# Optimization experiments

Hardware: AMD Instinct MI355X
Metric: run time of the kernel (lower is better)

The kernel has to match this reference:

```python
import jax, jax.numpy as jnp
import numpy as np

B, T = 64, 64
H = 256
CLIP = 0.2


def _conv(x, W, b, s):
    y = jax.lax.conv_general_dilated(x, W, (s, s), 'VALID',
                                     dimension_numbers=('NHWC', 'HWIO', 'NHWC'))
    return jax.nn.leaky_relu(y + b, negative_slope=0.2)


def _lstm(x, Wk, Wr, b):
    # keras LSTM, gate order i,f,g,o; x: (B,T,256) -> (B,T,256)
    h0 = jnp.zeros((x.shape[0], H), x.dtype)

    def step(carry, xt):
        h, c = carry
        z = xt @ Wk + h @ Wr + b
        i, f, g, o = jnp.split(z, 4, axis=-1)
        c = jax.nn.sigmoid(f) * c + jax.nn.sigmoid(i) * jnp.tanh(g)
        h = jax.nn.sigmoid(o) * jnp.tanh(c)
        return (h, c), h

    _, hs = jax.lax.scan(step, (h0, h0), jnp.swapaxes(x, 0, 1))
    return jnp.swapaxes(hs, 0, 1)


def setup_inputs():
    key = jax.random.key(0)
    ks = jax.random.split(key, 24)
    s = 0.05
    x = jax.random.normal(ks[0], (B, T, 13, 8, 8), jnp.float32)
    a_taken = jax.random.randint(ks[1], (B, T), 0, 36)
    mask = jax.random.randint(ks[2], (B, T, 4096), 0, 2).astype(jnp.int32)
    # taken actions must be legal (mask=1), as in real rollouts
    bi = jnp.repeat(jnp.arange(B), T)
    ti = jnp.tile(jnp.arange(T), B)
    mask = mask.at[bi, ti, a_taken.reshape(-1)].set(1)
    lg_prob_old = -jnp.abs(jax.random.normal(ks[3], (B, T), jnp.float32)) - 1.0
    GAE = jax.random.normal(ks[4], (B, T), jnp.float32)
    old_v_pred = jax.random.normal(ks[5], (B, T), jnp.float32)
    returns = jax.random.normal(ks[6], (B, T), jnp.float32)
    return {
        'x': x, 'mask': mask, 'lg_prob_old': lg_prob_old, 'a_taken': a_taken,
        'GAE': GAE, 'old_v_pred': old_v_pred, 'returns': returns,
        'W1': jax.random.normal(ks[7], (2, 2, 8, 16), jnp.float32) * s,
        'b1': jnp.zeros((16,), jnp.float32),
        'W2': jax.random.normal(ks[8], (2, 2, 16, 32), jnp.float32) * s,
        'b2': jnp.zeros((32,), jnp.float32),
        'W3': jax.random.normal(ks[9], (2, 2, 32, 64), jnp.float32) * s,
        'b3': jnp.zeros((64,), jnp.float32),
        'W4': jax.random.normal(ks[10], (1, 1, 64, 128), jnp.float32) * s,
        'b4': jnp.zeros((128,), jnp.float32),
        'lstm_k': jax.random.normal(ks[11], (256, 1024), jnp.float32) * s,
        'lstm_r': jax.random.normal(ks[12], (256, 1024), jnp.float32) * s,
        'lstm_b': jnp.zeros((1024,), jnp.float32),
        'pir_W': jax.random.normal(ks[13], (256, 36), jnp.float32) * s,
        'pir_b': jnp.zeros((36,), jnp.float32),
        'pim_W': jax.random.normal(ks[14], (256, 4096), jnp.float32) * s,
        'pim_b': jnp.zeros((4096,), jnp.float32),
        'v_W': jax.random.normal(ks[15], (256, 1), jnp.float32) * s,
        'v_b': jnp.zeros((1,), jnp.float32),
    }


def reference(x, mask, lg_prob_old, a_taken, GAE, old_v_pred, returns,
              W1, b1, W2, b2, W3, b3, W4, b4,
              lstm_k, lstm_r, lstm_b, pir_W, pir_b, pim_W, pim_b, v_W, v_b):
    Bn, Tn = x.shape[0], x.shape[1]
    h = x.reshape(Bn * Tn, 13, 8, 8)  # NHWC: H=13, W=8, C=8
    h = _conv(h, W1, b1, 2)  # (BT,6,4,16)
    h = _conv(h, W2, b2, 1)  # (BT,5,3,32)
    h = _conv(h, W3, b3, 2)  # (BT,2,1,64)
    h = _conv(h, W4, b4, 1)  # (BT,2,1,128)
    # keras Flatten(data_format='channels_first') permutes dim1 to last then flattens
    h = jnp.transpose(h, (0, 2, 3, 1)).reshape(Bn, Tn, -1)  # (B,T,256)
    lstm = _lstm(h, lstm_k, lstm_r, lstm_b).reshape(-1, H)  # (BT,256)

    pir = jax.nn.softmax(lstm @ pir_W + pir_b, axis=-1)  # (BT,36)
    maskf = mask.reshape(-1, 4096).astype(jnp.float32)
    pim = jax.nn.softmax(lstm @ pim_W + pim_b, axis=-1) * maskf
    scale = jnp.sum(pim, axis=1, keepdims=True)
    pim = pim / jnp.where(scale > 0, scale, jnp.ones_like(scale))  # (BT,4096)
    vpred = lstm @ v_W + v_b  # (BT,1)

    lg_old = lg_prob_old.reshape(-1)
    a = a_taken.reshape(-1)
    gae = GAE.reshape(-1)
    ovp = old_v_pred.reshape(-1)
    ret = returns.reshape(-1)
    gae = (gae - jnp.mean(gae)) / (jnp.std(gae) + 1e-8)

    t = jnp.arange(a.shape[0])
    p = jnp.where(t % 2 == 0, pir[t, a], pim[t, a])  # alternating heads
    lg_new = jnp.log(p)
    rt = jnp.exp(lg_new - lg_old)
    pg1 = -gae * rt
    pg2 = -gae * jnp.clip(rt, 1.0 - CLIP, 1.0 + CLIP)
    pg_loss = jnp.mean(jnp.maximum(pg1, pg2))

    # faithful to original TF: (BT,1) vpred broadcast against (BT,) -> (BT,BT)
    vpredclipped = ovp + jnp.clip(vpred - ovp, -CLIP, CLIP)
    vf1 = jnp.square(vpred - ret)
    vf2 = jnp.square(vpredclipped - ret)
    vf_loss = 0.5 * jnp.mean(jnp.maximum(vf1, vf2))

    pim_e = pim + (1.0 - maskf)
    entropy = -jnp.sum(pir * jnp.log(pir)) - jnp.sum(pim_e * jnp.log(pim_e))
    loss = pg_loss - entropy + vf_loss
    return (loss, pg_loss, entropy, vf_loss)
```

## Files before the change

### kernel.cpp

```cpp
#include <hip/hip_runtime.h>

typedef unsigned short u16;
typedef unsigned int   u32;

#define BT   4096
#define TSEQ 64
#define NB   64

typedef __attribute__((ext_vector_type(8))) short  short8;
typedef __attribute__((ext_vector_type(4))) float  f32x4;
typedef __attribute__((ext_vector_type(4))) int    i32x4;
typedef __attribute__((ext_vector_type(2))) _Float16 h2;

__device__ __forceinline__ float bf(u16 v) {
    u32 u = ((u32)v) << 16;
    return __builtin_bit_cast(float, u);
}
__device__ __forceinline__ u16 f2b(float f) {
    u32 u = __builtin_bit_cast(u32, f);
    return (u16)((u + 0x7fffu + ((u >> 16) & 1u)) >> 16);
}
__device__ __forceinline__ float lrelu(float x) { return x > 0.f ? x : 0.2f * x; }
__device__ __forceinline__ h2 i2h(int v) { return __builtin_bit_cast(h2, v); }
__device__ __forceinline__ float dot2(int hbits, int wbits, float acc) {
#if __has_builtin(__builtin_amdgcn_fdot2)
    return __builtin_amdgcn_fdot2(i2h(hbits), i2h(wbits), acc, false);
#else
    h2 a = i2h(hbits), b = i2h(wbits);
    return acc + (float)a.x * (float)b.x + (float)a.y * (float)b.y;
#endif
}
__device__ __forceinline__ float fsigm(float x) { return 1.f / (1.f + __expf(-x)); }
__device__ __forceinline__ float ftanh(float x) { return 1.f - 2.f / (__expf(2.f * x) + 1.f); }
__device__ __forceinline__ float ldf(const void* p, int i, int f32) {
    return f32 ? ((const float*)p)[i] : bf(((const u16*)p)[i]);
}
__device__ __forceinline__ u16 ldb(const void* p, int i, int f32) {
    return f32 ? f2b(((const float*)p)[i]) : ((const u16*)p)[i];
}

struct PrepPtrs {
    const void *x, *W1, *b1, *W2, *b2, *W3, *b3, *W4, *b4;
    const void *Wr, *Wk, *Wpim, *Wpir, *Wv;
    const u16* probe;
    u16 *featbf, *PF, *PBk, *PBpim, *PBpir;
    float* scal; int* flag;
};

#define PACK_BLKS 776
#define CONV_BLKS 2048

__global__ __launch_bounds__(256) void prep_kernel(PrepPtrs P)
{
    const int bid = blockIdx.x, tid = threadIdx.x;
    const int lane = tid & 63;
    u16 pv = P.probe[2 * lane];
    int e = (pv >> 7) & 0xFF;
    unsigned long long m = __ballot(pv == 0 || (e >= 100 && e <= 130));
    const int f32 = (__popcll(m) < 48) ? 1 : 0;

    if (bid == 0 && tid < 32) { P.scal[tid] = 0.f; if (tid == 0) *P.flag = f32; }

    if (bid < PACK_BLKS) {
        u16 t8[8];
        if (bid < 128) {
            int gid = bid * 256 + tid;
            int col = gid & 1023, oct = gid >> 10;
#pragma unroll
            for (int j = 0; j < 8; j++) {
                float f = ldf(P.Wr, (oct * 8 + j) * 1024 + col, f32);
                _Float16 h = (_Float16)f;
                t8[j] = __builtin_bit_cast(unsigned short, h);
            }
            *(int4*)&P.PF[((size_t)oct * 1024 + col) * 8] = *(int4*)t8;
        } else if (bid < 256) {
            int gid = (bid - 128) * 256 + tid;
            int col = gid & 1023, oct = gid >> 10;
#pragma unroll
            for (int j = 0; j < 8; j++) t8[j] = ldb(P.Wk, (oct * 8 + j) * 1024 + col, f32);
            *(int4*)&P.PBk[((((size_t)(oct >> 2) << 10) + col) * 4 + (oct & 3)) * 8] = *(int4*)t8;
        } else if (bid < 768) {
            int gid = (bid - 256) * 256 + tid;
            int col = gid & 4095, oct = gid >> 12;
#pragma unroll
            for (int j = 0; j < 8; j++) t8[j] = ldb(P.Wpim, (size_t)(oct * 8 + j) * 4096 + col, f32);
            *(int4*)&P.PBpim[((((size_t)(oct >> 2) << 12) + col) * 4 + (oct & 3)) * 8] = *(int4*)t8;
        } else {
            int gid = (bid - 768) * 256 + tid;
            int col = gid & 63, oct = gid >> 6;
#pragma unroll
            for (int j = 0; j < 8; j++) {
                int k = oct * 8 + j;
                u16 v = 0;
                if (col < 36)       v = ldb(P.Wpir, k * 36 + col, f32);
                else if (col == 36) v = ldb(P.Wv, k, f32);
                t8[j] = v;
            }
            *(int4*)&P.PBpir[(((size_t)(oct >> 2) * 64 + col) * 4 + (oct & 3)) * 8] = *(int4*)t8;
        }
        return;
    }

    __shared__ __align__(16) u16 wl[19184];
    __shared__ float xs[2][832];
    __shared__ float c1[2][384];
    __shared__ float c2[2][480];
    __shared__ float c3[2][128];
    const int pair = bid - PACK_BLKS;
    const int sub = tid >> 7, stid = tid & 127;
    const int bt = pair * 2 + sub;

    {
        const void* sp[8] = {P.W1, P.b1, P.W2, P.b2, P.W3, P.b3, P.W4, P.b4};
        const int   sn[8] = {512, 16, 2048, 32, 8192, 64, 8192, 128};
        int o = 0;
        for (int s = 0; s < 8; s++) {
            if (f32) {
                const float4* src = (const float4*)sp[s];
                for (int i = tid; i < (sn[s] >> 2); i += 256) {
                    float4 v = src[i];
                    ushort4 w;
                    w.x = f2b(v.x); w.y = f2b(v.y); w.z = f2b(v.z); w.w = f2b(v.w);
                    *(ushort4*)&wl[o + i * 4] = w;
                }
            } else {
                const int4* src = (const int4*)sp[s];
                for (int i = tid; i < (sn[s] >> 3); i += 256)
                    *(int4*)&wl[o + i * 8] = src[i];
            }
            o += sn[s];
        }
    }
    for (int i = stid; i < 832; i += 128) xs[sub][i] = ldf(P.x, bt * 832 + i, f32);
    __syncthreads();

    for (int idx = stid; idx < 96; idx += 128) {
        int pos = idx >> 2, g = idx & 3;
        int oh = pos >> 2, ow = pos & 3;
        float a0 = bf(wl[512 + g * 4]), a1 = bf(wl[513 + g * 4]),
              a2 = bf(wl[514 + g * 4]), a3 = bf(wl[515 + g * 4]);
        for (int kh = 0; kh < 2; kh++)
            for (int kw = 0; kw < 2; kw++)
#pragma unroll
                for (int ic = 0; ic < 8; ic++) {
                    float xv = xs[sub][(2 * oh + kh) * 64 + (2 * ow + kw) * 8 + ic];
                    ushort4 w = *(const ushort4*)&wl[((kh * 2 + kw) * 8 + ic) * 16 + g * 4];
                    a0 += xv * bf(w.x); a1 += xv * bf(w.y);
                    a2 += xv * bf(w.z); a3 += xv * bf(w.w);
                }
        c1[sub][pos * 16 + g * 4]     = lrelu(a0);
        c1[sub][pos * 16 + g * 4 + 1] = lrelu(a1);
        c1[sub][pos * 16 + g * 4 + 2] = lrelu(a2);
        c1[sub][pos * 16 + g * 4 + 3] = lrelu(a3);
    }
    __syncthreads();

    for (int idx = stid; idx < 120; idx += 128) {
        int pos = idx >> 3, g = idx & 7;
        int oh = pos / 3, ow = pos % 3;
        float a0 = bf(wl[2576 + g * 4]), a1 = bf(wl[2577 + g * 4]),
              a2 = bf(wl[2578 + g * 4]), a3 = bf(wl[2579 + g * 4]);
        for (int kh = 0; kh < 2; kh++)
            for (int kw = 0; kw < 2; kw++)
#pragma unroll
                for (int ic = 0; ic < 16; ic++) {
                    float xv = c1[sub][((oh + kh) * 4 + (ow + kw)) * 16 + ic];
                    ushort4 w = *(const ushort4*)&wl[528 + ((kh * 2 + kw) * 16 + ic) * 32 + g * 4];
                    a0 += xv * bf(w.x); a1 += xv * bf(w.y);
                    a2 += xv * bf(w.z); a3 += xv * bf(w.w);
                }
        c2[sub][pos * 32 + g * 4]     = lrelu(a0);
        c2[sub][pos * 32 + g * 4 + 1] = lrelu(a1);
        c2[sub][pos * 32 + g * 4 + 2] = lrelu(a2);
        c2[sub][pos * 32 + g * 4 + 3] = lrelu(a3);
    }
    __syncthreads();

    for (int idx = stid; idx < 32; idx += 128) {
        int oh = idx >> 4, g = idx & 15;
        float a0 = bf(wl[10800 + g * 4]), a1 = bf(wl[10801 + g * 4]),
              a2 = bf(wl[10802 + g * 4]), a3 = bf(wl[10803 + g * 4]);
        for (int kh = 0; kh < 2; kh++)
            for (int kw = 0; kw < 2; kw++)
#pragma unroll
                for (int ic = 0; ic < 32; ic++) {
                    float xv = c2[sub][((2 * oh + kh) * 3 + kw) * 32 + ic];
                    ushort4 w = *(const ushort4*)&wl[2608 + ((kh * 2 + kw) * 32 + ic) * 64 + g * 4];
                    a0 += xv * bf(w.x); a1 += xv * bf(w.y);
                    a2 += xv * bf(w.z); a3 += xv * bf(w.w);
                }
        c3[sub][oh * 64 + g * 4]     = lrelu(a0);
        c3[sub][oh * 64 + g * 4 + 1] = lrelu(a1);
        c3[sub][oh * 64 + g * 4 + 2] = lrelu(a2);
        c3[sub][oh * 64 + g * 4 + 3] = lrelu(a3);
    }
    __syncthreads();

    for (int idx = stid; idx < 64; idx += 128) {
        int oh = idx >> 5, g = idx & 31;
        float a0 = bf(wl[19056 + g * 4]), a1 = bf(wl[19057 + g * 4]),
              a2 = bf(wl[19058 + g * 4]), a3 = bf(wl[19059 + g * 4]);
#pragma unroll
        for (int ic = 0; ic < 64; ic++) {
            float xv = c3[sub][oh * 64 + ic];
            ushort4 w = *(const ushort4*)&wl[10864 + ic * 128 + g * 4];
            a0 += xv * bf(w.x); a1 += xv * bf(w.y);
            a2 += xv * bf(w.z); a3 += xv * bf(w.w);
        }
        P.featbf[bt * 256 + (g * 4 + 0) * 2 + oh] = f2b(lrelu(a0));
        P.featbf[bt * 256 + (g * 4 + 1) * 2 + oh] = f2b(lrelu(a1));
        P.featbf[bt * 256 + (g * 4 + 2) * 2 + oh] = f2b(lrelu(a2));
        P.featbf[bt * 256 + (g * 4 + 3) * 2 + oh] = f2b(lrelu(a3));
    }
}

__global__ __launch_bounds__(256) void gemm_zx(
    const u16* __restrict__ Abf, const u16* __restrict__ PB,
    const void* __restrict__ bias, const int* __restrict__ flag,
    float* __restrict__ out)
{
    __shared__ __align__(16) u16 As[16 * 264];
    const int mb = blockIdx.y, nb = blockIdx.x, tid = threadIdx.x;
    const int f32 = *flag;
    const int m0 = mb * 16;
    {
        int row = tid >> 4, part = tid & 15;
        const f32x4* src = (const f32x4*)&Abf[(size_t)(m0 + row) * 256 + part * 16];
        f32x4 v0 = src[0], v1 = src[1];
        *(f32x4*)&As[row * 264 + part * 16] = v0;
        *(f32x4*)&As[row * 264 + part * 16 + 8] = v1;
    }
    __syncthreads();
    const int wv = tid >> 6, lane = tid & 63;
    const int colw = lane & 15, q = lane >> 4;
    const int n = nb * 64 + wv * 16 + colw;
    f32x4 acc = {0.f, 0.f, 0.f, 0.f};
#pragma unroll
    for (int kt = 0; kt < 8; kt++) {
        short8 a = *(const short8*)&As[colw * 264 + kt * 32 + q * 8];
        short8 b = *(const short8*)&PB[((((size_t)kt << 10) + n) * 4 + q) * 8];
        acc = __builtin_amdgcn_mfma_f32_16x16x32_bf16(a, b, acc, 0, 0, 0);
    }
    const float bj = ldf(bias, n, f32);
#pragma unroll
    for (int r = 0; r < 4; r++) {
        int row = q * 4 + r;
        out[(size_t)(m0 + row) * 1024 + n] = acc[r] + bj;
    }
}

#define NREG 12
#define NLDS4 4
__global__ __launch_bounds__(512)
__attribute__((amdgpu_waves_per_eu(2, 2)))
void lstm_kernel(
    const float* __restrict__ zx, const u16* __restrict__ PF,
    u16* __restrict__ hseqbf)
{
    __shared__ __align__(16) u16 h16[2][264];
    __shared__ __align__(16) int4 wlds[2][NLDS4][4][256];
    const int b = blockIdx.x, tid = threadIdx.x;
    const int c = tid >> 1, kh = tid & 1;
    const int4* Pw = (const int4*)PF;

    int4 wr[NREG][4];
#pragma unroll
    for (int o = 0; o < NREG; o++)
#pragma unroll
        for (int g = 0; g < 4; g++)
            wr[o][g] = Pw[(size_t)(kh * 16 + o) * 1024 + g * 256 + c];
#pragma unroll
    for (int o = 0; o < NLDS4; o++)
#pragma unroll
        for (int g = 0; g < 4; g++)
            wlds[kh][o][g][c] = Pw[(size_t)(kh * 16 + NREG + o) * 1024 + g * 256 + c];

    if (tid < 128) ((u32*)h16[0])[tid] = 0u;
    float cst = 0.f;
    const size_t z0 = (size_t)b * TSEQ * 1024;
    float zxv0 = zx[z0 + c],       zxv1 = zx[z0 + 256 + c];
    float zxv2 = zx[z0 + 512 + c], zxv3 = zx[z0 + 768 + c];
    __syncthreads();

    for (int t = 0; t < TSEQ; t++) {
        const u16* hb = h16[t & 1];
        float a0 = 0.f, a1 = 0.f, a2 = 0.f, a3 = 0.f;
#pragma unroll
        for (int o = 0; o < NREG; o++) {
            int4 hv = *(const int4*)&hb[(kh * 16 + o) * 8];
            a0 = dot2(hv.x, wr[o][0].x, a0); a0 = dot2(hv.y, wr[o][0].y, a0);
            a0 = dot2(hv.z, wr[o][0].z, a0); a0 = dot2(hv.w, wr[o][0].w, a0);
            a1 = dot2(hv.x, wr[o][1].x, a1); a1 = dot2(hv.y, wr[o][1].y, a1);
            a1 = dot2(hv.z, wr[o][1].z, a1); a1 = dot2(hv.w, wr[o][1].w, a1);
            a2 = dot2(hv.x, wr[o][2].x, a2); a2 = dot2(hv.y, wr[o][2].y, a2);
            a2 = dot2(hv.z, wr[o][2].z, a2); a2 = dot2(hv.w, wr[o][2].w, a2);
            a3 = dot2(hv.x, wr[o][3].x, a3); a3 = dot2(hv.y, wr[o][3].y, a3);
            a3 = dot2(hv.z, wr[o][3].z, a3); a3 = dot2(hv.w, wr[o][3].w, a3);
        }
#pragma unroll
        for (int o = 0; o < NLDS4; o++) {
            int4 hv = *(const int4*)&hb[(kh * 16 + NREG + o) * 8];
            int4 w0 = wlds[kh][o][0][c];
            int4 w1 = wlds[kh][o][1][c];
            int4 w2 = wlds[kh][o][2][c];
            int4 w3 = wlds[kh][o][3][c];
            a0 = dot2(hv.x, w0.x, a0); a0 = dot2(hv.y, w0.y, a0);
            a0 = dot2(hv.z, w0.z, a0); a0 = dot2(hv.w, w0.w, a0);
            a1 = dot2(hv.x, w1.x, a1); a1 = dot2(hv.y, w1.y, a1);
            a1 = dot2(hv.z, w1.z, a1); a1 = dot2(hv.w, w1.w, a1);
            a2 = dot2(hv.x, w2.x, a2); a2 = dot2(hv.y, w2.y, a2);
            a2 = dot2(hv.z, w2.z, a2); a2 = dot2(hv.w, w2.w, a2);
            a3 = dot2(hv.x, w3.x, a3); a3 = dot2(hv.y, w3.y, a3);
            a3 = dot2(hv.z, w3.z, a3); a3 = dot2(hv.w, w3.w, a3);
        }
        float zi = a0 + __shfl_xor(a0, 1, 64) + zxv0;
        float zf = a1 + __shfl_xor(a1, 1, 64) + zxv1;
        float zg = a2 + __shfl_xor(a2, 1, 64) + zxv2;
        float zo = a3 + __shfl_xor(a3, 1, 64) + zxv3;
        if (t + 1 < TSEQ) {
            const size_t zr = z0 + (size_t)(t + 1) * 1024;
            zxv0 = zx[zr + c];       zxv1 = zx[zr + 256 + c];
            zxv2 = zx[zr + 512 + c]; zxv3 = zx[zr + 768 + c];
        }
        float ig = fsigm(zi), fg = fsigm(zf), og = fsigm(zo);
        float gg = ftanh(zg);
        cst = fg * cst + ig * gg;
        float h = og * ftanh(cst);
        if (kh == 0) h16[(t & 1) ^ 1][c] = __builtin_bit_cast(unsigned short, (_Float16)h);
        else         hseqbf[(size_t)b * (TSEQ * 256) + t * 256 + c] = f2b(h);
        __syncthreads();
    }
}

__global__ __launch_bounds__(256) void pir_kernel(
    const u16* __restrict__ Abf, const u16* __restrict__ PB,
    const void* __restrict__ pir_b, const void* __restrict__ v_b,
    const int* __restrict__ flag, const int* __restrict__ a_taken,
    float* __restrict__ entpir, float* __restrict__ ppira, float* __restrict__ vpred)
{
    __shared__ __align__(16) u16 As[64 * 264];
    const int tid = threadIdx.x;
    const int wv = tid >> 6, lane = tid & 63;
    const int colw = lane & 15, q = lane >> 4;
    const int f32 = *flag;
    const int m0 = blockIdx.x * 64;

    for (int idx = tid; idx < 1024; idx += 256) {
        int row = idx >> 4, part = idx & 15;
        const f32x4* src = (const f32x4*)&Abf[(size_t)(m0 + row) * 256 + part * 16];
        f32x4 v0 = src[0], v1 = src[1];
        *(f32x4*)&As[row * 264 + part * 16] = v0;
        *(f32x4*)&As[row * 264 + part * 16 + 8] = v1;
    }
    __syncthreads();
    f32x4 acc[4];
#pragma unroll
    for (int nt = 0; nt < 4; nt++) acc[nt] = (f32x4){0.f, 0.f, 0.f, 0.f};
#pragma unroll
    for (int kt = 0; kt < 8; kt++) {
        short8 a = *(const short8*)&As[(wv * 16 + colw) * 264 + kt * 32 + q * 8];
#pragma unroll
        for (int nt = 0; nt < 4; nt++) {
            short8 b = *(const short8*)&PB[((((size_t)kt * 64) + nt * 16 + colw) * 4 + q) * 8];
            acc[nt] = __builtin_amdgcn_mfma_f32_16x16x32_bf16(a, b, acc[nt], 0, 0, 0);
        }
    }
    float* zq = (float*)&As[wv * 4224];
#pragma unroll
    for (int nt = 0; nt < 4; nt++) {
        int col = nt * 16 + colw;
        float bj = (col < 36) ? ldf(pir_b, col, f32)
                              : (col == 36 ? ldf(v_b, 0, f32) : 0.f);
#pragma unroll
        for (int r = 0; r < 4; r++)
            zq[(q * 4 + r) * 65 + col] = acc[nt][r] + bj;
    }
    if (lane < 16) {
        int R = m0 + wv * 16 + lane;
        const float* zrow = &zq[lane * 65];
        float Z = 0.f, U = 0.f;
        for (int cc = 0; cc < 36; cc++) {
            float z = zrow[cc];
            float ev = __expf(z);
            Z += ev; U += ev * z;
        }
        entpir[R] = logf(Z) - U / Z;
        ppira[R]  = __expf(zrow[a_taken[R]]) / Z;
        vpred[R]  = zrow[36];
    }
}

__global__ __launch_bounds__(256) void pim_kernel(
    const u16* __restrict__ Abf, const u16* __restrict__ PB,
    const void* __restrict__ pim_b, const int* __restrict__ flag,
    const int* __restrict__ mask, const int* __restrict__ a_taken,
    float* __restrict__ partS, float* __restrict__ partU, float* __restrict__ za)
{
    __shared__ __align__(16) u16 As[32 * 264];
    __shared__ float redS[4][32], redU[4][32];
    const int nb = blockIdx.x, mb = blockIdx.y, tid = threadIdx.x;
    const int wv = tid >> 6, lane = tid & 63;
    const int colw = lane & 15, q = lane >> 4;
    const int f32 = *flag;
    const int m0 = mb * 32;

    for (int idx = tid; idx < 512; idx += 256) {
        int row = idx >> 4, part = idx & 15;
        const f32x4* src = (const f32x4*)&Abf[(size_t)(m0 + row) * 256 + part * 16];
        f32x4 v0 = src[0], v1 = src[1];
        *(f32x4*)&As[row * 264 + part * 16] = v0;
        *(f32x4*)&As[row * 264 + part * 16 + 8] = v1;
    }
    __syncthreads();
    const int n = nb * 64 + wv * 16 + colw;
    f32x4 acc0 = {0.f, 0.f, 0.f, 0.f}, acc1 = {0.f, 0.f, 0.f, 0.f};
#pragma unroll
    for (int kt = 0; kt < 8; kt++) {
        short8 b = *(const short8*)&PB[((((size_t)kt << 12) + n) * 4 + q) * 8];
        short8 a0 = *(const short8*)&As[colw * 264 + kt * 32 + q * 8];
        short8 a1 = *(const short8*)&As[(16 + colw) * 264 + kt * 32 + q * 8];
        acc0 = __builtin_amdgcn_mfma_f32_16x16x32_bf16(a0, b, acc0, 0, 0, 0);
        acc1 = __builtin_amdgcn_mfma_f32_16x16x32_bf16(a1, b, acc1, 0, 0, 0);
    }
    const float bj = ldf(pim_b, n, f32);
#pragma unroll
    for (int half = 0; half < 2; half++) {
        const f32x4& acc = half ? acc1 : acc0;
        float sv[4], uv[4];
#pragma unroll
        for (int r = 0; r < 4; r++) {
            int row = m0 + half * 16 + q * 4 + r;
            float z = acc[r] + bj;
            int mm = mask[(size_t)row * 4096 + n];
            float ev = __expf(z);
            sv[r] = mm ? ev : 0.f;
            uv[r] = mm ? ev * z : 0.f;
            if (n == a_taken[row]) za[row] = z;
        }
#pragma unroll
        for (int r = 0; r < 4; r++) {
            for (int off = 1; off < 16; off <<= 1) {
                sv[r] += __shfl_xor(sv[r], off, 16);
                uv[r] += __shfl_xor(uv[r], off, 16);
            }
            if (colw == 0) {
                redS[wv][half * 16 + q * 4 + r] = sv[r];
                redU[wv][half * 16 + q * 4 + r] = uv[r];
            }
        }
    }
    __syncthreads();
    if (tid < 32) {
        float S = redS[0][tid] + redS[1][tid] + redS[2][tid] + redS[3][tid];
        float U = redU[0][tid] + redU[1][tid] + redU[2][tid] + redU[3][tid];
        partS[(size_t)(m0 + tid) * 64 + nb] = S;
        partU[(size_t)(m0 + tid) * 64 + nb] = U;
    }
}

#define TAIL_BLOCKS (16 + 256)
__global__ __launch_bounds__(256) void tail_kernel(
    const float* __restrict__ partS, const float* __restrict__ partU,
    const float* __restrict__ za,
    const float* __restrict__ entpir, const float* __restrict__ ppira,
    const float* __restrict__ vpred,
    const void* __restrict__ lgold, const void* __restrict__ gae,
    const void* __restrict__ ovp, const void* __restrict__ ret,
    float* __restrict__ scal, const int* __restrict__ flag,
    void* __restrict__ out)
{
    const int bid = blockIdx.x, tid = threadIdx.x;
    const int f32 = *flag;
    __shared__ float sh[8];
    __shared__ float mst[2];
    if (bid < 16) {
        const int r = bid * 256 + tid;
        float S = 0.f, U = 0.f;
#pragma unroll
        for (int t2 = 0; t2 < 64; t2++) {
            S += partS[(size_t)r * 64 + t2];
            U += partU[(size_t)r * 64 + t2];
        }
        float entpim = logf(S) - U / S;
        float ppima = __expf(za[r]) / S;
        float s = 0.f, s2 = 0.f;
        if (f32) {
            const float* gp = (const float*)gae;
            for (int i = tid; i < BT; i += 256) { float v = gp[i]; s += v; s2 += v * v; }
        } else {
            const u16* gp = (const u16*)gae;
            for (int i = tid; i < BT; i += 256) { float v = bf(gp[i]); s += v; s2 += v * v; }
        }
        for (int off = 32; off; off >>= 1) {
            s += __shfl_down(s, off, 64); s2 += __shfl_down(s2, off, 64);
        }
        if ((tid & 63) == 0) { sh[tid >> 6] = s; sh[4 + (tid >> 6)] = s2; }
        __syncthreads();
        if (tid == 0) {
            float Sa = sh[0] + sh[1] + sh[2] + sh[3];
            float S2a = sh[4] + sh[5] + sh[6] + sh[7];
            float mean = Sa / (float)BT;
            float var = S2a / (float)BT - mean * mean;
            mst[0] = mean; mst[1] = sqrtf(fmaxf(var, 0.f));
        }
        __syncthreads();
        float mean = mst[0], sd = mst[1];
        float p = (r & 1) ? ppima : ppira[r];
        float ln = logf(p);
        float rt = __expf(ln - ldf(lgold, r, f32));
        float g = (ldf(gae, r, f32) - mean) / (sd + 1e-8f);
        float rtc = fminf(fmaxf(rt, 0.8f), 1.2f);
        float pg = fmaxf(-g * rt, -g * rtc);
        float e12 = entpir[r] + entpim;
        for (int off = 32; off; off >>= 1) {
            pg += __shfl_down(pg, off, 64);
            e12 += __shfl_down(e12, off, 64);
        }
        if ((tid & 63) == 0) {
            atomicAdd(&scal[2], pg);
            atomicAdd(&scal[3], e12);
        }
    } else {
        const int i0 = (bid - 16) * 16;
        float s = 0.f;
        if (f32) {
            const float* rp = (const float*)ret;
            const float* op = (const float*)ovp;
            for (int rr = 0; rr < 16; rr++) {
                float vp = vpred[i0 + rr];
                for (int j = tid; j < BT; j += 256) {
                    float r2 = rp[j], o = op[j];
                    float d = fminf(fmaxf(vp - o, -0.2f), 0.2f);
                    float v1 = vp - r2;    v1 *= v1;
                    float v2 = o + d - r2; v2 *= v2;
                    s += fmaxf(v1, v2);
                }
            }
        } else {
            const u16* rp = (const u16*)ret;
            const u16* op = (const u16*)ovp;
            for (int rr = 0; rr < 16; rr++) {
                float vp = vpred[i0 + rr];
                for (int j = tid; j < BT; j += 256) {
                    float r2 = bf(rp[j]), o = bf(op[j]);
                    float d = fminf(fmaxf(vp - o, -0.2f), 0.2f);
                    float v1 = vp - r2;    v1 *= v1;
                    float v2 = o + d - r2; v2 *= v2;
                    s += fmaxf(v1, v2);
                }
            }
        }
        for (int off = 32; off; off >>= 1) s += __shfl_down(s, off, 64);
        if ((tid & 63) == 0) sh[tid >> 6] = s;
        __syncthreads();
        if (tid == 0) atomicAdd(&scal[5], sh[0] + sh[1] + sh[2] + sh[3]);
    }
    __threadfence();
    __syncthreads();
    if (tid == 0) {
        unsigned old = atomicAdd((unsigned int*)&scal[8], 1u);
        if (old == TAIL_BLOCKS - 1) {
            __threadfence();
            float pgs = atomicAdd(&scal[2], 0.f);
            float ents = atomicAdd(&scal[3], 0.f);
            float vfs = atomicAdd(&scal[5], 0.f);
            float pg = pgs / (float)BT;
            float vf = 0.5f * vfs / ((float)BT * (float)BT);
            float loss = pg - ents + vf;
            if (f32) {
                float* o = (float*)out;
                o[0] = loss; o[1] = pg; o[2] = ents; o[3] = vf;
            } else {
                u16* o = (u16*)out;
                o[0] = f2b(loss); o[1] = f2b(pg); o[2] = f2b(ents); o[3] = f2b(vf);
            }
        }
    }
}

extern "C" void kernel_launch(void* const* d_in, const int* in_sizes, int n_in,
                              void* d_out, int out_size, void* d_ws, size_t ws_size,
                              hipStream_t stream)
{
    const int* mask = (const int*)d_in[1];
    const int* a_tk = (const int*)d_in[3];

    float* p = (float*)d_ws;
    u16*   featbf = (u16*)p;            p += 524288;
    float* zx     = p;                  p += 4194304;
    u16*   hseqbf = (u16*)p;            p += 524288;
    u16*   PF     = (u16*)p;            p += 131072;
    u16*   PBk    = (u16*)p;            p += 131072;
    u16*   PBpim  = (u16*)p;            p += 524288;
    u16*   PBpir  = (u16*)p;            p += 8192;
    float* scal   = p;                  p += 32;
    int*   flag   = (int*)p;            p += 4;
    float* partS  = p;                  p += 262144;
    float* partU  = p;                  p += 262144;
    float* za     = p;                  p += 4096;
    float* entpir = p;                  p += 4096;
    float* ppira  = p;                  p += 4096;
    float* vpred  = p;                  p += 4096;

    PrepPtrs P;
    P.x = d_in[0];
    P.W1 = d_in[7];  P.b1 = d_in[8];
    P.W2 = d_in[9];  P.b2 = d_in[10];
    P.W3 = d_in[11]; P.b3 = d_in[12];
    P.W4 = d_in[13]; P.b4 = d_in[14];
    P.Wk = d_in[15]; P.Wr = d_in[16];
    P.Wpir = d_in[18]; P.Wpim = d_in[20]; P.Wv = d_in[22];
    P.probe = (const u16*)d_in[15];
    P.featbf = featbf; P.PF = PF; P.PBk = PBk; P.PBpim = PBpim; P.PBpir = PBpir;
    P.scal = scal; P.flag = flag;

    prep_kernel<<<PACK_BLKS + CONV_BLKS, 256, 0, stream>>>(P);
    gemm_zx<<<dim3(16, 256), 256, 0, stream>>>(featbf, PBk, d_in[17], flag, zx);
    lstm_kernel<<<NB, 512, 0, stream>>>(zx, PF, hseqbf);
    pir_kernel<<<64, 256, 0, stream>>>(hseqbf, PBpir, d_in[19], d_in[23], flag,
                                       a_tk, entpir, ppira, vpred);
    pim_kernel<<<dim3(64, 128), 256, 0, stream>>>(hseqbf, PBpim, d_in[21], flag,
                                                  mask, a_tk, partS, partU, za);
    tail_kernel<<<TAIL_BLOCKS, 256, 0, stream>>>(
        partS, partU, za, entpir, ppira, vpred,
        d_in[2], d_in[4], d_in[5], d_in[6], scal, flag, (void*)d_out);
}
```

Measured before the change: 435.1 us.

## Compute LSTM recurrent matvec with f16 MFMA instead of fdot2 chains

The per-step recurrent h·Wr product moves from per-thread fdot2 accumulation to 16x16x32 f16 MFMA. The h vector is broadcast across the A rows and only row 0 of each result is used. Weight k-tiles are spread across three places: three tiles pinned in AGPRs, two tiles in a 128KB LDS buffer, and three tiles re-read from global memory every timestep. Gate pre-activations go through shared memory to 256 threads that do the cell update, which adds an extra barrier per step. The aim is to raise matvec throughput on the serial recurrence, but the global weight reloads and 16x redundant MFMA rows may leave the loop latency-bound.

```diff
diff --git a/kernel.cpp b/kernel.cpp
--- a/kernel.cpp
+++ b/kernel.cpp
@@ -10,6 +10,7 @@
 typedef __attribute__((ext_vector_type(8))) short  short8;
 typedef __attribute__((ext_vector_type(4))) float  f32x4;
 typedef __attribute__((ext_vector_type(4))) int    i32x4;
+typedef __attribute__((ext_vector_type(8))) _Float16 half8;
 typedef __attribute__((ext_vector_type(2))) _Float16 h2;
 
 __device__ __forceinline__ float bf(u16 v) {
@@ -22,14 +23,6 @@
 }
 __device__ __forceinline__ float lrelu(float x) { return x > 0.f ? x : 0.2f * x; }
 __device__ __forceinline__ h2 i2h(int v) { return __builtin_bit_cast(h2, v); }
-__device__ __forceinline__ float dot2(int hbits, int wbits, float acc) {
-#if __has_builtin(__builtin_amdgcn_fdot2)
-    return __builtin_amdgcn_fdot2(i2h(hbits), i2h(wbits), acc, false);
-#else
-    h2 a = i2h(hbits), b = i2h(wbits);
-    return acc + (float)a.x * (float)b.x + (float)a.y * (float)b.y;
-#endif
-}
 __device__ __forceinline__ float fsigm(float x) { return 1.f / (1.f + __expf(-x)); }
 __device__ __forceinline__ float ftanh(float x) { return 1.f - 2.f / (__expf(2.f * x) + 1.f); }
 __device__ __forceinline__ float ldf(const void* p, int i, int f32) {
@@ -37,6 +30,9 @@
 }
 __device__ __forceinline__ u16 ldb(const void* p, int i, int f32) {
     return f32 ? f2b(((const float*)p)[i]) : ((const u16*)p)[i];
+}
+__device__ __forceinline__ f32x4 mfma16(half8 a, half8 b, f32x4 c) {
+    return __builtin_amdgcn_mfma_f32_16x16x32_f16(a, b, c, 0, 0, 0);
 }
 
 struct PrepPtrs {
@@ -249,8 +245,6 @@
     }
 }
 
-#define NREG 12
-#define NLDS4 4
 __global__ __launch_bounds__(512)
 __attribute__((amdgpu_waves_per_eu(2, 2)))
 void lstm_kernel(
@@ -258,76 +252,83 @@
     u16* __restrict__ hseqbf)
 {
     __shared__ __align__(16) u16 h16[2][264];
-    __shared__ __align__(16) int4 wlds[2][NLDS4][4][256];
+    __shared__ float zp[1024];
+    __shared__ __align__(16) u16 wl2[65536];
     const int b = blockIdx.x, tid = threadIdx.x;
-    const int c = tid >> 1, kh = tid & 1;
-    const int4* Pw = (const int4*)PF;
-
-    int4 wr[NREG][4];
-#pragma unroll
-    for (int o = 0; o < NREG; o++)
-#pragma unroll
-        for (int g = 0; g < 4; g++)
-            wr[o][g] = Pw[(size_t)(kh * 16 + o) * 1024 + g * 256 + c];
-#pragma unroll
-    for (int o = 0; o < NLDS4; o++)
-#pragma unroll
-        for (int g = 0; g < 4; g++)
-            wlds[kh][o][g][c] = Pw[(size_t)(kh * 16 + NREG + o) * 1024 + g * 256 + c];
-
-    if (tid < 128) ((u32*)h16[0])[tid] = 0u;
+    const int wv = tid >> 6, lane = tid & 63;
+    const int colw = lane & 15, q = lane >> 4;
+    const int n0 = wv * 128 + colw;
+
+    i32x4 ba[8][3];
+#pragma unroll
+    for (int nt = 0; nt < 8; nt++)
+#pragma unroll
+        for (int kt = 0; kt < 3; kt++)
+            ba[nt][kt] = *(const i32x4*)&PF[((size_t)(kt * 4 + q) * 1024 + n0 + nt * 16) * 8];
+#pragma unroll
+    for (int nt = 0; nt < 8; nt++)
+#pragma unroll
+        for (int kt = 0; kt < 3; kt++)
+            asm volatile("" : "+a"(ba[nt][kt]));
+
+    for (int i = tid; i < 8192; i += 512)
+        *(int4*)&wl2[(size_t)i * 8] = *(const int4*)&PF[(size_t)(12 * 1024 + i) * 8];
+
+    if (tid < 132) { ((u32*)h16[0])[tid] = 0u; }
     float cst = 0.f;
     const size_t z0 = (size_t)b * TSEQ * 1024;
-    float zxv0 = zx[z0 + c],       zxv1 = zx[z0 + 256 + c];
-    float zxv2 = zx[z0 + 512 + c], zxv3 = zx[z0 + 768 + c];
+    float zxv0 = 0.f, zxv1 = 0.f, zxv2 = 0.f, zxv3 = 0.f;
+    if (tid < 256) {
+        zxv0 = zx[z0 + tid];       zxv1 = zx[z0 + 256 + tid];
+        zxv2 = zx[z0 + 512 + tid]; zxv3 = zx[z0 + 768 + tid];
+    }
     __syncthreads();
 
     for (int t = 0; t < TSEQ; t++) {
         const u16* hb = h16[t & 1];
-        float a0 = 0.f, a1 = 0.f, a2 = 0.f, a3 = 0.f;
-#pragma unroll
-        for (int o = 0; o < NREG; o++) {
-            int4 hv = *(const int4*)&hb[(kh * 16 + o) * 8];
-            a0 = dot2(hv.x, wr[o][0].x, a0); a0 = dot2(hv.y, wr[o][0].y, a0);
-            a0 = dot2(hv.z, wr[o][0].z, a0); a0 = dot2(hv.w, wr[o][0].w, a0);
-            a1 = dot2(hv.x, wr[o][1].x, a1); a1 = dot2(hv.y, wr[o][1].y, a1);
-            a1 = dot2(hv.z, wr[o][1].z, a1); a1 = dot2(hv.w, wr[o][1].w, a1);
-            a2 = dot2(hv.x, wr[o][2].x, a2); a2 = dot2(hv.y, wr[o][2].y, a2);
-            a2 = dot2(hv.z, wr[o][2].z, a2); a2 = dot2(hv.w, wr[o][2].w, a2);
-            a3 = dot2(hv.x, wr[o][3].x, a3); a3 = dot2(hv.y, wr[o][3].y, a3);
-            a3 = dot2(hv.z, wr[o][3].z, a3); a3 = dot2(hv.w, wr[o][3].w, a3);
-        }
-#pragma unroll
-        for (int o = 0; o < NLDS4; o++) {
-            int4 hv = *(const int4*)&hb[(kh * 16 + NREG + o) * 8];
-            int4 w0 = wlds[kh][o][0][c];
-            int4 w1 = wlds[kh][o][1][c];
-            int4 w2 = wlds[kh][o][2][c];
-            int4 w3 = wlds[kh][o][3][c];
-            a0 = dot2(hv.x, w0.x, a0); a0 = dot2(hv.y, w0.y, a0);
-            a0 = dot2(hv.z, w0.z, a0); a0 = dot2(hv.w, w0.w, a0);
-            a1 = dot2(hv.x, w1.x, a1); a1 = dot2(hv.y, w1.y, a1);
-            a1 = dot2(hv.z, w1.z, a1); a1 = dot2(hv.w, w1.w, a1);
-            a2 = dot2(hv.x, w2.x, a2); a2 = dot2(hv.y, w2.y, a2);
-            a2 = dot2(hv.z, w2.z, a2); a2 = dot2(hv.w, w2.w, a2);
-            a3 = dot2(hv.x, w3.x, a3); a3 = dot2(hv.y, w3.y, a3);
-            a3 = dot2(hv.z, w3.z, a3); a3 = dot2(hv.w, w3.w, a3);
-        }
-        float zi = a0 + __shfl_xor(a0, 1, 64) + zxv0;
-        float zf = a1 + __shfl_xor(a1, 1, 64) + zxv1;
-        float zg = a2 + __shfl_xor(a2, 1, 64) + zxv2;
-        float zo = a3 + __shfl_xor(a3, 1, 64) + zxv3;
-        if (t + 1 < TSEQ) {
-            const size_t zr = z0 + (size_t)(t + 1) * 1024;
-            zxv0 = zx[zr + c];       zxv1 = zx[zr + 256 + c];
-            zxv2 = zx[zr + 512 + c]; zxv3 = zx[zr + 768 + c];
-        }
-        float ig = fsigm(zi), fg = fsigm(zf), og = fsigm(zo);
-        float gg = ftanh(zg);
-        cst = fg * cst + ig * gg;
-        float h = og * ftanh(cst);
-        if (kh == 0) h16[(t & 1) ^ 1][c] = __builtin_bit_cast(unsigned short, (_Float16)h);
-        else         hseqbf[(size_t)b * (TSEQ * 256) + t * 256 + c] = f2b(h);
+        half8 af[8];
+#pragma unroll
+        for (int kt = 0; kt < 8; kt++)
+            af[kt] = *(const half8*)&hb[kt * 32 + q * 8];
+
+        float zv[8];
+#pragma unroll
+        for (int nt = 0; nt < 8; nt++) {
+            const int n = n0 + nt * 16;
+            f32x4 acc = {0.f, 0.f, 0.f, 0.f};
+            acc = mfma16(af[0], __builtin_bit_cast(half8, ba[nt][0]), acc);
+            acc = mfma16(af[1], __builtin_bit_cast(half8, ba[nt][1]), acc);
+            acc = mfma16(af[2], __builtin_bit_cast(half8, ba[nt][2]), acc);
+            acc = mfma16(af[3], *(const half8*)&wl2[((size_t)(0 * 4 + q) * 1024 + n) * 8], acc);
+            acc = mfma16(af[4], *(const half8*)&wl2[((size_t)(1 * 4 + q) * 1024 + n) * 8], acc);
+            acc = mfma16(af[5], *(const half8*)&PF[((size_t)(20 + q) * 1024 + n) * 8], acc);
+            acc = mfma16(af[6], *(const half8*)&PF[((size_t)(24 + q) * 1024 + n) * 8], acc);
+            acc = mfma16(af[7], *(const half8*)&PF[((size_t)(28 + q) * 1024 + n) * 8], acc);
+            zv[nt] = acc[0];
+        }
+        if (q == 0) {
+#pragma unroll
+            for (int nt = 0; nt < 8; nt++) zp[n0 + nt * 16] = zv[nt];
+        }
+        __syncthreads();
+
+        if (tid < 256) {
+            float zi = zp[tid] + zxv0;
+            float zf = zp[256 + tid] + zxv1;
+            float zg = zp[512 + tid] + zxv2;
+            float zo = zp[768 + tid] + zxv3;
+            if (t + 1 < TSEQ) {
+                const size_t zr = z0 + (size_t)(t + 1) * 1024;
+                zxv0 = zx[zr + tid];       zxv1 = zx[zr + 256 + tid];
+                zxv2 = zx[zr + 512 + tid]; zxv3 = zx[zr + 768 + tid];
+            }
+            float ig = fsigm(zi), fg = fsigm(zf), og = fsigm(zo);
+            float gg = ftanh(zg);
+            cst = fg * cst + ig * gg;
+            float h = og * ftanh(cst);
+            h16[(t & 1) ^ 1][tid] = __builtin_bit_cast(unsigned short, (_Float16)h);
+            hseqbf[(size_t)b * (TSEQ * 256) + t * 256 + tid] = f2b(h);
+        }
         __syncthreads();
     }
 }
```

Result: slower. 528.0 us (+21.3%).
